# Kernel optimization log

Hardware: AMD Instinct MI355X
Metric: run time of the kernel (lower is better)

The kernel has to match this reference:

```python
import jax, jax.numpy as jnp
import numpy as np

N_STATE = 64
N_OBS = 32
N_IN = 16
T = 1024
DT = 0.01

# Dopri5 Butcher tableau (same as diffrax.Dopri5)
_A_TAB = [
    [],
    [1/5],
    [3/40, 9/40],
    [44/45, -56/15, 32/9],
    [19372/6561, -25360/2187, 64448/6561, -212/729],
    [9017/3168, -355/33, 46732/5247, 49/176, -5103/18656],
    [35/384, 0.0, 500/1113, 125/192, -2187/6784, 11/84],
]
_C_TAB = [0.0, 1/5, 3/10, 4/5, 8/9, 1.0, 1.0]
_B_TAB = [35/384, 0.0, 500/1113, 125/192, -2187/6784, 11/84, 0.0]


def setup_inputs() -> dict:
    key = jax.random.key(0)
    ks = jax.random.split(key, 6)
    ts = jnp.arange(T, dtype=jnp.float32) * DT
    ys = jax.random.normal(ks[0], (T, N_OBS), jnp.float32)
    us = jax.random.normal(ks[1], (T, N_IN), jnp.float32)
    # stable system matrix so the Riccati ODE stays bounded
    A = 0.1 * jax.random.normal(ks[2], (N_STATE, N_STATE), jnp.float32) - jnp.eye(N_STATE, dtype=jnp.float32)
    B = 0.1 * jax.random.normal(ks[3], (N_STATE, N_IN), jnp.float32)
    C = 0.1 * jax.random.normal(ks[4], (N_OBS, N_STATE), jnp.float32)
    x0 = jax.random.normal(ks[5], (N_STATE,), jnp.float32)
    P0 = jnp.eye(N_STATE, dtype=jnp.float32)
    Q = 0.01 * jnp.eye(N_STATE, dtype=jnp.float32)
    R = 0.1 * jnp.eye(N_OBS, dtype=jnp.float32)
    return {"ts": ts, "ys": ys, "us": us, "A": A, "B": B, "C": C,
            "x0": x0, "P0": P0, "Q": Q, "R": R}


def reference(ts, ys, us, A, B, C, x0, P0, Q, R):
    h = ts[1] - ts[0]  # constant step == save spacing (dt0)
    nT = ys.shape[0]
    Rinv = jnp.linalg.inv(R)  # R is constant; original inverts it each rhs eval
    Ct = C.T

    def interp(arr, t):
        # linear interpolation on the uniform grid ts
        s = (t - ts[0]) / h
        i0 = jnp.clip(jnp.floor(s).astype(jnp.int32), 0, nT - 2)
        w = s - i0.astype(s.dtype)
        return arr[i0] * (1.0 - w) + arr[i0 + 1] * w

    def rhs(t, x, P):
        PCtRi = P @ Ct @ Rinv                      # Kalman gain K, [n,p]
        dP = A @ P + P @ A.T + Q - PCtRi @ (C @ P)  # Riccati ODE
        dx = A @ x + B @ interp(us, t) + PCtRi @ (interp(ys, t) - C @ x)
        return dx, dP

    def step(carry, t):
        x, P = carry
        kx, kP = [], []
        for i in range(7):  # fixed 7-stage RK, unrolled
            xi, Pi = x, P
            for j, aij in enumerate(_A_TAB[i]):
                if aij != 0.0:
                    xi = xi + (h * aij) * kx[j]
                    Pi = Pi + (h * aij) * kP[j]
            dx, dP = rhs(t + _C_TAB[i] * h, xi, Pi)
            kx.append(dx)
            kP.append(dP)
        xn, Pn = x, P
        for i, bi in enumerate(_B_TAB):
            if bi != 0.0:
                xn = xn + (h * bi) * kx[i]
                Pn = Pn + (h * bi) * kP[i]
        return (xn, Pn), xn

    (_, _), xs = jax.lax.scan(step, (x0, P0), ts[:-1])
    return jnp.concatenate([x0[None], xs], axis=0)  # [T, n] filtered states
```

## Files before the change

### kernel.cpp

```cpp
#include <hip/hip_runtime.h>

typedef float f32x4 __attribute__((ext_vector_type(4)));
typedef short s16x8 __attribute__((ext_vector_type(8)));
typedef short s16x4 __attribute__((ext_vector_type(4)));

namespace kf {
constexpr int TN = 1024, NS = 64, NO = 32, NI = 16;
constexpr int PP = 72;
constexpr int PK = 40;
constexpr int PKP = 72;

constexpr float ATAB[6][5] = {
  {0.f,0.f,0.f,0.f,0.f},
  {(float)(1.0/5.0),0.f,0.f,0.f,0.f},
  {(float)(3.0/40.0),(float)(9.0/40.0),0.f,0.f,0.f},
  {(float)(44.0/45.0),(float)(-56.0/15.0),(float)(32.0/9.0),0.f,0.f},
  {(float)(19372.0/6561.0),(float)(-25360.0/2187.0),(float)(64448.0/6561.0),(float)(-212.0/729.0),0.f},
  {(float)(9017.0/3168.0),(float)(-355.0/33.0),(float)(46732.0/5247.0),(float)(49.0/176.0),(float)(-5103.0/18656.0)},
};
constexpr float CTAB[6] = {0.f,(float)(1.0/5.0),(float)(3.0/10.0),(float)(4.0/5.0),(float)(8.0/9.0),1.f};
constexpr float BW0=(float)(35.0/384.0), BW2=(float)(500.0/1113.0), BW3=(float)(125.0/192.0),
                BW4=(float)(-2187.0/6784.0), BW5=(float)(11.0/84.0);

struct ShB {
  unsigned short Pib[64*PP];
  unsigned short Ab [64*PP];
  unsigned short Cb [32*PP];
  unsigned short RCb[32*PP];
  unsigned short KKb[64*PK];
  unsigned short GTb[64*PK];
  float Bf[64*16];
  float XV[2][64];
  float CXR[32];
  float BUB[2][64];
  float FAC[32];
  int HYP;
};
constexpr size_t SH_BASE  = (sizeof(ShB) + 255) & ~size_t(255);
constexpr size_t SH_TOTAL = SH_BASE + size_t(5*64*PKP)*4;
}
using namespace kf;

__device__ inline float bf2f(unsigned short u){
  unsigned int x = ((unsigned int)u) << 16; return __builtin_bit_cast(float, x);
}
__device__ inline unsigned short f2bf(float f){
  unsigned int x = __builtin_bit_cast(unsigned int, f);
  return (unsigned short)((x + 0x7fffu + ((x >> 16) & 1u)) >> 16);
}
__device__ inline unsigned int pack2bf(float a, float b){
  return (unsigned int)f2bf(a) | ((unsigned int)f2bf(b) << 16);
}
__device__ inline s16x8 load_frag(const unsigned short* arr, int pitch, int row0, int k0, int hyp){
  const int l = (int)(threadIdx.x & 63), lc = l & 15, lg = l >> 4;
  const unsigned short* p = arr + (row0 + lc) * pitch + k0;
  if ((hyp & 1) == 0) {
    return *(const s16x8*)(p + lg * 8);
  } else {
    s16x4 a = *(const s16x4*)(p + lg * 4);
    s16x4 b = *(const s16x4*)(p + 16 + lg * 4);
    s16x8 r; r[0]=a[0]; r[1]=a[1]; r[2]=a[2]; r[3]=a[3]; r[4]=b[0]; r[5]=b[1]; r[6]=b[2]; r[7]=b[3];
    return r;
  }
}
__device__ inline f32x4 MF(s16x8 a, s16x8 b, f32x4 c, int hyp){
  if (hyp & 2) return __builtin_amdgcn_mfma_f32_16x16x32_bf16(b, a, c, 0, 0, 0);
  return __builtin_amdgcn_mfma_f32_16x16x32_bf16(a, b, c, 0, 0, 0);
}
template<int HYP>
__device__ __forceinline__ s16x8 load_fragT(const unsigned short* arr, int pitch, int row0, int k0){
  const int l = (int)(threadIdx.x & 63), lc = l & 15, lg = l >> 4;
  const unsigned short* p = arr + (row0 + lc) * pitch + k0;
  if constexpr ((HYP & 1) == 0) {
    return *(const s16x8*)(p + lg * 8);
  } else {
    s16x4 a = *(const s16x4*)(p + lg * 4);
    s16x4 b = *(const s16x4*)(p + 16 + lg * 4);
    s16x8 r; r[0]=a[0]; r[1]=a[1]; r[2]=a[2]; r[3]=a[3]; r[4]=b[0]; r[5]=b[1]; r[6]=b[2]; r[7]=b[3];
    return r;
  }
}
template<int HYP>
__device__ __forceinline__ f32x4 MFT(s16x8 a, s16x8 b, f32x4 c){
  if constexpr ((HYP & 2) != 0) return __builtin_amdgcn_mfma_f32_16x16x32_bf16(b, a, c, 0, 0, 0);
  else                          return __builtin_amdgcn_mfma_f32_16x16x32_bf16(a, b, c, 0, 0, 0);
}
__device__ inline float dot8(s16x8 v, f32x4 a, f32x4 b){
  return bf2f(v[0])*a.x + bf2f(v[1])*a.y + bf2f(v[2])*a.z + bf2f(v[3])*a.w
       + bf2f(v[4])*b.x + bf2f(v[5])*b.y + bf2f(v[6])*b.z + bf2f(v[7])*b.w;
}
__device__ inline float dot4bf(s16x4 v, f32x4 a){
  return bf2f(v[0])*a.x + bf2f(v[1])*a.y + bf2f(v[2])*a.z + bf2f(v[3])*a.w;
}

template<int HYP>
__device__ __forceinline__ void scan_body(ShB& sh, float* __restrict__ KPL,
    const float* __restrict__ ts, const float* __restrict__ ys, const float* __restrict__ us,
    const float* __restrict__ x0g, const float* __restrict__ P0g, const float* __restrict__ Qg,
    float* __restrict__ out)
{
  const int tid = (int)threadIdx.x;
  const int w = tid >> 6, l = tid & 63;
  const int lc = l & 15, lg = l >> 4;
  const int sr = w & 3, ch = w >> 2;
  const int xrow = tid >> 3, xpart = tid & 7;
  const int cq = tid >> 4, cpart = tid & 15;

  const float h = ts[1] - ts[0];
  f32x4 z4 = {0.f,0.f,0.f,0.f};
  f32x4 Pfr[2], Qfr[2], APd[2], APT[2];
  s16x8 aA[2], aRC[2], aC[2];
  float XRr, kx0=0.f,kx1=0.f,kx2=0.f,kx3=0.f,kx4=0.f;
  float y1, y2;
  #pragma unroll
  for (int c2 = 0; c2 < 2; ++c2) { Pfr[c2]=z4; Qfr[c2]=z4; APd[c2]=z4; APT[c2]=z4; }

  #pragma unroll
  for (int c2 = 0; c2 < 2; ++c2)
    #pragma unroll
    for (int r = 0; r < 4; ++r) {
      int row = 16*sr + 4*lg + r, col = 16*(2*ch + c2) + lc;
      Pfr[c2][r] = P0g[row*64 + col];
      Qfr[c2][r] = Qg [row*64 + col];
    }
  #pragma unroll
  for (int kb = 0; kb < 2; ++kb) {
    aA [kb] = load_fragT<HYP>(sh.Ab,  PP, 16*sr, 32*kb);
    aRC[kb] = load_fragT<HYP>(sh.RCb, PP, 16*ch, 32*kb);
    aC [kb] = load_fragT<HYP>(sh.Cb,  PP, 16*ch, 32*kb);
  }
  XRr = x0g[xrow];
  if (tid < 64) {
    out[tid] = x0g[tid];
    const f32x4* bf4 = (const f32x4*)&sh.Bf[tid*16];
    const f32x4* up4 = (const f32x4*)us;
    float bu = 0.f;
    #pragma unroll
    for (int m4 = 0; m4 < 4; ++m4) {
      f32x4 b = bf4[m4], u = up4[m4];
      bu += b.x*u.x + b.y*u.y + b.z*u.z + b.w*u.w;
    }
    sh.BUB[0][tid] = bu;
  }
  y1 = ys[cq]; y2 = ys[NO + cq];
  __syncthreads();

  for (int t = 0; t < TN - 1; ++t) {
    #pragma unroll
    for (int st = 0; st < 6; ++st) {
      const int par = st & 1, prv = par ^ 1;
      if (t > 0 || st > 0) {
        float kx;
        {
          s16x8 a0 = *(const s16x8*)&sh.Ab[xrow*PP + 8*xpart];
          f32x4 xa = *(const f32x4*)&sh.XV[prv][8*xpart];
          f32x4 xb = *(const f32x4*)&sh.XV[prv][8*xpart + 4];
          kx = dot8(a0, xa, xb);
          s16x4 kkv = *(const s16x4*)&sh.KKb[xrow*PK + 4*xpart];
          f32x4 cxv = *(const f32x4*)&sh.CXR[4*xpart];
          kx += dot4bf(kkv, cxv);
        }
        kx += __shfl_xor(kx, 1);
        kx += __shfl_xor(kx, 2);
        kx += __shfl_xor(kx, 4);
        if (st == 0) {
          kx += sh.BUB[t & 1][xrow];
        } else {
          const float cp = CTAB[st-1];
          kx += (1.f - cp) * sh.BUB[t & 1][xrow] + cp * sh.BUB[(t + 1) & 1][xrow];
        }
        if (st == 0) {
          float xn = XRr + h*(BW0*kx0 + BW2*kx2 + BW3*kx3 + BW4*kx4 + BW5*kx);
          XRr = xn;
          if (xpart == 0) { out[t*64 + xrow] = xn; sh.XV[par][xrow] = xn; }
        } else {
          float xi = XRr + (h * ATAB[st][st-1]) * kx;
          if (st >= 2 && ATAB[st][0] != 0.f) xi += (h * ATAB[st][0]) * kx0;
          if (st >= 3 && ATAB[st][1] != 0.f) xi += (h * ATAB[st][1]) * kx1;
          if (st >= 4 && ATAB[st][2] != 0.f) xi += (h * ATAB[st][2]) * kx2;
          if (st >= 5 && ATAB[st][3] != 0.f) xi += (h * ATAB[st][3]) * kx3;
          if (st == 1) kx0 = kx; else if (st == 2) kx1 = kx;
          else if (st == 3) kx2 = kx; else if (st == 4) kx3 = kx; else kx4 = kx;
          if (xpart == 0) sh.XV[par][xrow] = xi;
        }
      } else {
        if (xpart == 0) sh.XV[0][xrow] = XRr;
      }
      if (t > 0 || st > 0) {
        s16x8 am = load_fragT<HYP>(sh.KKb, PK, 16*sr, 0);
        #pragma unroll
        for (int c2 = 0; c2 < 2; ++c2) {
          const int ct = 2*ch + c2;
          s16x8 bg = load_fragT<HYP>(sh.GTb, PK, 16*ct, 0);
          f32x4 M = MFT<HYP>(am, bg, z4);
          f32x4 kPv;
          #pragma unroll
          for (int r = 0; r < 4; ++r) kPv[r] = APd[c2][r] + APT[c2][r] - M[r];
          float* kbase = &KPL[(size_t)(16*ct + lc) * PKP + 16*sr + 4*lg];
          f32x4 x;
          if (st == 0) {
            f32x4 k0v = *(const f32x4*)(kbase + 0*64*PKP);
            f32x4 k2v = *(const f32x4*)(kbase + 2*64*PKP);
            f32x4 k3v = *(const f32x4*)(kbase + 3*64*PKP);
            f32x4 k4v = *(const f32x4*)(kbase + 4*64*PKP);
            #pragma unroll
            for (int r = 0; r < 4; ++r)
              Pfr[c2][r] += h * (BW0*k0v[r] + BW2*k2v[r] + BW3*k3v[r]
                               + BW4*k4v[r] + BW5*kPv[r] + Qfr[c2][r]);
            x = Pfr[c2];
          } else {
            *(f32x4*)(kbase + (size_t)(st-1)*64*PKP) = kPv;
            #pragma unroll
            for (int r = 0; r < 4; ++r)
              x[r] = Pfr[c2][r] + (h * CTAB[st]) * Qfr[c2][r] + (h * ATAB[st][st-1]) * kPv[r];
            if (st >= 2) { f32x4 kv = *(const f32x4*)(kbase + 0*64*PKP);
              #pragma unroll
              for (int r = 0; r < 4; ++r) x[r] += (h * ATAB[st][0]) * kv[r]; }
            if (st >= 3) { f32x4 kv = *(const f32x4*)(kbase + 1*64*PKP);
              #pragma unroll
              for (int r = 0; r < 4; ++r) x[r] += (h * ATAB[st][1]) * kv[r]; }
            if (st >= 4) { f32x4 kv = *(const f32x4*)(kbase + 2*64*PKP);
              #pragma unroll
              for (int r = 0; r < 4; ++r) x[r] += (h * ATAB[st][2]) * kv[r]; }
            if (st >= 5) { f32x4 kv = *(const f32x4*)(kbase + 3*64*PKP);
              #pragma unroll
              for (int r = 0; r < 4; ++r) x[r] += (h * ATAB[st][3]) * kv[r]; }
          }
          uint2 pk; pk.x = pack2bf(x[0], x[1]); pk.y = pack2bf(x[2], x[3]);
          *(uint2*)&sh.Pib[(16*ct + lc)*PP + 16*sr + 4*lg] = pk;
        }
      } else {
        #pragma unroll
        for (int c2 = 0; c2 < 2; ++c2) {
          const int ct = 2*ch + c2;
          uint2 pk; pk.x = pack2bf(Pfr[c2][0], Pfr[c2][1]); pk.y = pack2bf(Pfr[c2][2], Pfr[c2][3]);
          *(uint2*)&sh.Pib[(16*ct + lc)*PP + 16*sr + 4*lg] = pk;
        }
      }
      __syncthreads();
      {
        s16x8 aPi0 = load_fragT<HYP>(sh.Pib, PP, 16*sr, 0);
        s16x8 aPi1 = load_fragT<HYP>(sh.Pib, PP, 16*sr, 32);
        #pragma unroll
        for (int c2 = 0; c2 < 2; ++c2) {
          const int ct = 2*ch + c2;
          s16x8 bP0 = load_fragT<HYP>(sh.Pib, PP, 16*ct, 0);
          s16x8 bP1 = load_fragT<HYP>(sh.Pib, PP, 16*ct, 32);
          s16x8 bA0 = load_fragT<HYP>(sh.Ab,  PP, 16*ct, 0);
          s16x8 bA1 = load_fragT<HYP>(sh.Ab,  PP, 16*ct, 32);
          APd[c2] = MFT<HYP>(aA[1], bP1, MFT<HYP>(aA[0], bP0, z4));
          APT[c2] = MFT<HYP>(aPi1, bA1, MFT<HYP>(aPi0, bA0, z4));
        }
        f32x4 aK = MFT<HYP>(aRC[1], aPi1, MFT<HYP>(aRC[0], aPi0, z4));
        uint2 pkk; pkk.x = pack2bf(aK[0], aK[1]); pkk.y = pack2bf(aK[2], aK[3]);
        *(uint2*)&sh.KKb[(16*sr + lc)*PK + 16*ch + 4*lg] = pkk;
        f32x4 aG = MFT<HYP>(aC[1], aPi1, MFT<HYP>(aC[0], aPi0, z4));
        uint2 pkg; pkg.x = pack2bf(aG[0], aG[1]); pkg.y = pack2bf(aG[2], aG[3]);
        *(uint2*)&sh.GTb[(16*sr + lc)*PK + 16*ch + 4*lg] = pkg;
      }
      {
        s16x4 cvv = *(const s16x4*)&sh.Cb[cq*PP + 4*cpart];
        f32x4 xv = *(const f32x4*)&sh.XV[par][4*cpart];
        float cx = dot4bf(cvv, xv);
        cx += __shfl_xor(cx, 1);
        cx += __shfl_xor(cx, 2);
        cx += __shfl_xor(cx, 4);
        cx += __shfl_xor(cx, 8);
        if (cpart == 0) {
          float yc = (1.f - CTAB[st]) * y1 + CTAB[st] * y2;
          sh.CXR[cq] = yc - cx;
        }
      }
      if (st == 0 && tid < 64) {
        const f32x4* bf4 = (const f32x4*)&sh.Bf[tid*16];
        const f32x4* up4 = (const f32x4*)(us + (size_t)(t + 1)*NI);
        float bu = 0.f;
        #pragma unroll
        for (int m4 = 0; m4 < 4; ++m4) {
          f32x4 b = bf4[m4], u = up4[m4];
          bu += b.x*u.x + b.y*u.y + b.z*u.z + b.w*u.w;
        }
        sh.BUB[(t + 1) & 1][tid] = bu;
      }
      __syncthreads();
    }
    y1 = y2;
    if (t + 2 < TN) y2 = ys[(size_t)(t + 2)*NO + cq];
  }

  {
    constexpr int tb = (TN - 1) & 1;
    float kx;
    {
      s16x8 a0 = *(const s16x8*)&sh.Ab[xrow*PP + 8*xpart];
      f32x4 xa = *(const f32x4*)&sh.XV[1][8*xpart];
      f32x4 xb = *(const f32x4*)&sh.XV[1][8*xpart + 4];
      kx = dot8(a0, xa, xb);
      s16x4 kkv = *(const s16x4*)&sh.KKb[xrow*PK + 4*xpart];
      f32x4 cxv = *(const f32x4*)&sh.CXR[4*xpart];
      kx += dot4bf(kkv, cxv);
    }
    kx += __shfl_xor(kx, 1);
    kx += __shfl_xor(kx, 2);
    kx += __shfl_xor(kx, 4);
    kx += sh.BUB[tb][xrow];
    if (xpart == 0) {
      float xn = XRr + h*(BW0*kx0 + BW2*kx2 + BW3*kx3 + BW4*kx4 + BW5*kx);
      out[(TN - 1)*64 + xrow] = xn;
    }
  }
}

__global__ __launch_bounds__(512, 1)
void kf_mfma8(const float* __restrict__ ts, const float* __restrict__ ys,
              const float* __restrict__ us, const float* __restrict__ Ag,
              const float* __restrict__ Bg, const float* __restrict__ Cg,
              const float* __restrict__ x0g, const float* __restrict__ P0g,
              const float* __restrict__ Qg, const float* __restrict__ Rg,
              float* __restrict__ out)
{
  extern __shared__ char dsm[];
  ShB& sh = *(ShB*)dsm;
  float* KPL = (float*)(dsm + SH_BASE);
  float* GJ  = KPL;
  const int tid = (int)threadIdx.x;
  const int wv = tid >> 6;
  const int lc = tid & 15, lg = (tid & 63) >> 4;

  for (int idx = tid; idx < 64*64; idx += 512) sh.Ab[(idx>>6)*PP + (idx&63)] = f2bf(Ag[idx]);
  for (int idx = tid; idx < 32*64; idx += 512) sh.Cb[(idx>>6)*PP + (idx&63)] = f2bf(Cg[idx]);
  for (int idx = tid; idx < 64*16; idx += 512) sh.Bf[idx] = Bg[idx];
  for (int idx = tid; idx < 32*64; idx += 512) {
    int r = idx >> 6, c = idx & 63;
    GJ[idx] = (c < 32) ? Rg[r*32 + c] : ((c - 32) == r ? 1.f : 0.f);
  }
  __syncthreads();
  for (int k2 = 0; k2 < 32; ++k2) {
    if (tid < 32) sh.FAC[tid] = GJ[tid*64 + k2];
    __syncthreads();
    const float pinv = 1.f / sh.FAC[k2];
    float oldv[4], vk[4];
    #pragma unroll
    for (int s = 0; s < 4; ++s) {
      int idx = tid + s*512;
      oldv[s] = GJ[idx];
      vk[s]   = GJ[k2*64 + (idx & 63)];
    }
    __syncthreads();
    #pragma unroll
    for (int s = 0; s < 4; ++s) {
      int idx = tid + s*512, i = idx >> 6;
      GJ[idx] = (i == k2) ? (oldv[s] * pinv) : (oldv[s] - sh.FAC[i] * (vk[s] * pinv));
    }
    __syncthreads();
  }
  for (int idx = tid; idx < 32*64; idx += 512) {
    int q = idx >> 6, k = idx & 63;
    float a = 0.f;
    for (int p = 0; p < 32; ++p) a += GJ[q*64 + 32 + p] * Cg[p*64 + k];
    sh.RCb[q*PP + k] = f2bf(a);
  }
  __syncthreads();
  __shared__ float Xref[256];
  if (tid < 256) {
    int r = tid >> 4, c = tid & 15;
    float a = 0.f;
    for (int k = 0; k < 32; ++k) a += bf2f(sh.Ab[r*PP + k]) * bf2f(sh.Ab[(16 + c)*PP + k]);
    Xref[tid] = a;
  }
  if (tid == 0) sh.HYP = -1;
  __syncthreads();
  for (int hh = 0; hh < 4; ++hh) {
    if (wv == 0) {
      s16x8 af = load_frag(sh.Ab, PP, 0, 0, hh);
      s16x8 bf = load_frag(sh.Ab, PP, 16, 0, hh);
      f32x4 z = {0.f,0.f,0.f,0.f};
      f32x4 d = MF(af, bf, z, hh);
      int ok = 1;
      #pragma unroll
      for (int r = 0; r < 4; ++r) {
        float rf = Xref[(lg*4 + r)*16 + lc];
        ok &= (fabsf(d[r] - rf) <= 1e-3f + 1e-2f * fabsf(rf)) ? 1 : 0;
      }
      if (__all(ok) && tid == 0) { if (sh.HYP < 0) sh.HYP = hh; }
    }
    __syncthreads();
  }
  const int sHyp = (sh.HYP < 0) ? 0 : sh.HYP;

  switch (sHyp) {
    case 0: scan_body<0>(sh, KPL, ts, ys, us, x0g, P0g, Qg, out); break;
    case 1: scan_body<1>(sh, KPL, ts, ys, us, x0g, P0g, Qg, out); break;
    case 2: scan_body<2>(sh, KPL, ts, ys, us, x0g, P0g, Qg, out); break;
    default: scan_body<3>(sh, KPL, ts, ys, us, x0g, P0g, Qg, out); break;
  }
}

extern "C" void kernel_launch(void* const* d_in, const int* in_sizes, int n_in,
                              void* d_out, int out_size, void* d_ws, size_t ws_size,
                              hipStream_t stream) {
  (void)in_sizes; (void)n_in; (void)out_size; (void)d_ws; (void)ws_size;
  const float* ts  = (const float*)d_in[0];
  const float* ys  = (const float*)d_in[1];
  const float* us  = (const float*)d_in[2];
  const float* A   = (const float*)d_in[3];
  const float* B   = (const float*)d_in[4];
  const float* C   = (const float*)d_in[5];
  const float* x0  = (const float*)d_in[6];
  const float* P0  = (const float*)d_in[7];
  const float* Q   = (const float*)d_in[8];
  const float* R   = (const float*)d_in[9];
  (void)hipFuncSetAttribute(reinterpret_cast<const void*>(kf_mfma8),
                            hipFuncAttributeMaxDynamicSharedMemorySize, (int)SH_TOTAL);
  hipLaunchKernelGGL(kf_mfma8, dim3(1), dim3(512), SH_TOTAL, stream,
                     ts, ys, us, A, B, C, x0, P0, Q, R, (float*)d_out);
}
```

Measured before the change: 8.897 ms.

## Fold state-vector updates into MFMA tiles as an extra padded row of P

```diff
diff --git a/kernel.cpp b/kernel.cpp
--- a/kernel.cpp
+++ b/kernel.cpp
@@ -23,16 +23,15 @@
                 BW4=(float)(-2187.0/6784.0), BW5=(float)(11.0/84.0);
 
 struct ShB {
-  unsigned short Pib[64*PP];
+  unsigned short Pib[80*PP];
   unsigned short Ab [64*PP];
   unsigned short Cb [32*PP];
   unsigned short RCb[32*PP];
   unsigned short KKb[64*PK];
-  unsigned short GTb[64*PK];
+  unsigned short GTb[80*PK];
   float Bf[64*16];
-  float XV[2][64];
-  float CXR[32];
   float BUB[2][64];
+  float KXL[5][64];
   float FAC[32];
   int HYP;
 };
@@ -85,13 +84,6 @@
   if constexpr ((HYP & 2) != 0) return __builtin_amdgcn_mfma_f32_16x16x32_bf16(b, a, c, 0, 0, 0);
   else                          return __builtin_amdgcn_mfma_f32_16x16x32_bf16(a, b, c, 0, 0, 0);
 }
-__device__ inline float dot8(s16x8 v, f32x4 a, f32x4 b){
-  return bf2f(v[0])*a.x + bf2f(v[1])*a.y + bf2f(v[2])*a.z + bf2f(v[3])*a.w
-       + bf2f(v[4])*b.x + bf2f(v[5])*b.y + bf2f(v[6])*b.z + bf2f(v[7])*b.w;
-}
-__device__ inline float dot4bf(s16x4 v, f32x4 a){
-  return bf2f(v[0])*a.x + bf2f(v[1])*a.y + bf2f(v[2])*a.z + bf2f(v[3])*a.w;
-}
 
 template<int HYP>
 __device__ __forceinline__ void scan_body(ShB& sh, float* __restrict__ KPL,
@@ -103,17 +95,18 @@
   const int w = tid >> 6, l = tid & 63;
   const int lc = l & 15, lg = l >> 4;
   const int sr = w & 3, ch = w >> 2;
-  const int xrow = tid >> 3, xpart = tid & 7;
-  const int cq = tid >> 4, cpart = tid & 15;
+  const int rowbase = 16*sr + 4*lg;
+  const bool isx = (ch == 0);
+  const bool isg = (sr == 3);
 
   const float h = ts[1] - ts[0];
   f32x4 z4 = {0.f,0.f,0.f,0.f};
-  f32x4 Pfr[2], Qfr[2], APd[2], APT[2];
-  s16x8 aA[2], aRC[2], aC[2];
-  float XRr, kx0=0.f,kx1=0.f,kx2=0.f,kx3=0.f,kx4=0.f;
-  float y1, y2;
+  f32x4 Pfr[2], Qfr[2], APd[2], APT[2], APdX, XRv;
+  s16x8 aA[2], aRC[2], aC[2], bA[2][2];
+  f32x4 y1v = z4, y2v = z4;
   #pragma unroll
   for (int c2 = 0; c2 < 2; ++c2) { Pfr[c2]=z4; Qfr[c2]=z4; APd[c2]=z4; APT[c2]=z4; }
+  APdX = z4;
 
   #pragma unroll
   for (int c2 = 0; c2 < 2; ++c2)
@@ -128,10 +121,18 @@
     aA [kb] = load_fragT<HYP>(sh.Ab,  PP, 16*sr, 32*kb);
     aRC[kb] = load_fragT<HYP>(sh.RCb, PP, 16*ch, 32*kb);
     aC [kb] = load_fragT<HYP>(sh.Cb,  PP, 16*ch, 32*kb);
-  }
-  XRr = x0g[xrow];
+    #pragma unroll
+    for (int c2 = 0; c2 < 2; ++c2)
+      bA[c2][kb] = load_fragT<HYP>(sh.Ab, PP, 16*(2*ch + c2), 32*kb);
+  }
+  XRv = *(const f32x4*)&x0g[rowbase];
+  if (isg) {
+    y1v = *(const f32x4*)&ys[16*ch + 4*lg];
+    y2v = *(const f32x4*)&ys[NO + 16*ch + 4*lg];
+  }
   if (tid < 64) {
     out[tid] = x0g[tid];
+    sh.Pib[64*PP + tid] = f2bf(x0g[tid]);
     const f32x4* bf4 = (const f32x4*)&sh.Bf[tid*16];
     const f32x4* up4 = (const f32x4*)us;
     float bu = 0.f;
@@ -142,52 +143,17 @@
     }
     sh.BUB[0][tid] = bu;
   }
-  y1 = ys[cq]; y2 = ys[NO + cq];
+  for (int idx = tid; idx < 15*PP; idx += 512) sh.Pib[65*PP + idx] = 0;
+  if (tid < PP - 64) sh.Pib[64*PP + 64 + tid] = 0;
+  for (int idx = tid; idx < 16*PK; idx += 512) sh.GTb[64*PK + idx] = 0;
   __syncthreads();
 
   for (int t = 0; t < TN - 1; ++t) {
     #pragma unroll
     for (int st = 0; st < 6; ++st) {
-      const int par = st & 1, prv = par ^ 1;
+      s16x8 am;
       if (t > 0 || st > 0) {
-        float kx;
-        {
-          s16x8 a0 = *(const s16x8*)&sh.Ab[xrow*PP + 8*xpart];
-          f32x4 xa = *(const f32x4*)&sh.XV[prv][8*xpart];
-          f32x4 xb = *(const f32x4*)&sh.XV[prv][8*xpart + 4];
-          kx = dot8(a0, xa, xb);
-          s16x4 kkv = *(const s16x4*)&sh.KKb[xrow*PK + 4*xpart];
-          f32x4 cxv = *(const f32x4*)&sh.CXR[4*xpart];
-          kx += dot4bf(kkv, cxv);
-        }
-        kx += __shfl_xor(kx, 1);
-        kx += __shfl_xor(kx, 2);
-        kx += __shfl_xor(kx, 4);
-        if (st == 0) {
-          kx += sh.BUB[t & 1][xrow];
-        } else {
-          const float cp = CTAB[st-1];
-          kx += (1.f - cp) * sh.BUB[t & 1][xrow] + cp * sh.BUB[(t + 1) & 1][xrow];
-        }
-        if (st == 0) {
-          float xn = XRr + h*(BW0*kx0 + BW2*kx2 + BW3*kx3 + BW4*kx4 + BW5*kx);
-          XRr = xn;
-          if (xpart == 0) { out[t*64 + xrow] = xn; sh.XV[par][xrow] = xn; }
-        } else {
-          float xi = XRr + (h * ATAB[st][st-1]) * kx;
-          if (st >= 2 && ATAB[st][0] != 0.f) xi += (h * ATAB[st][0]) * kx0;
-          if (st >= 3 && ATAB[st][1] != 0.f) xi += (h * ATAB[st][1]) * kx1;
-          if (st >= 4 && ATAB[st][2] != 0.f) xi += (h * ATAB[st][2]) * kx2;
-          if (st >= 5 && ATAB[st][3] != 0.f) xi += (h * ATAB[st][3]) * kx3;
-          if (st == 1) kx0 = kx; else if (st == 2) kx1 = kx;
-          else if (st == 3) kx2 = kx; else if (st == 4) kx3 = kx; else kx4 = kx;
-          if (xpart == 0) sh.XV[par][xrow] = xi;
-        }
-      } else {
-        if (xpart == 0) sh.XV[0][xrow] = XRr;
-      }
-      if (t > 0 || st > 0) {
-        s16x8 am = load_fragT<HYP>(sh.KKb, PK, 16*sr, 0);
+        am = load_fragT<HYP>(sh.KKb, PK, 16*sr, 0);
         #pragma unroll
         for (int c2 = 0; c2 < 2; ++c2) {
           const int ct = 2*ch + c2;
@@ -229,6 +195,46 @@
           uint2 pk; pk.x = pack2bf(x[0], x[1]); pk.y = pack2bf(x[2], x[3]);
           *(uint2*)&sh.Pib[(16*ct + lc)*PP + 16*sr + 4*lg] = pk;
         }
+        if (isx) {
+          s16x8 bgX = load_fragT<HYP>(sh.GTb, PK, 64, 0);
+          f32x4 MX = MFT<HYP>(am, bgX, z4);
+          f32x4 kx = APdX + MX;
+          {
+            f32x4 bu1 = *(const f32x4*)&sh.BUB[t & 1][rowbase];
+            if (st == 0) {
+              kx += bu1;
+            } else {
+              const float cp = CTAB[st-1];
+              if (cp != 0.f) {
+                f32x4 bu2 = *(const f32x4*)&sh.BUB[(t + 1) & 1][rowbase];
+                kx += (1.f - cp) * bu1 + cp * bu2;
+              } else {
+                kx += bu1;
+              }
+            }
+          }
+          f32x4 xiv;
+          if (st == 0) {
+            f32x4 k0 = *(const f32x4*)&sh.KXL[0][rowbase];
+            f32x4 k2 = *(const f32x4*)&sh.KXL[2][rowbase];
+            f32x4 k3 = *(const f32x4*)&sh.KXL[3][rowbase];
+            f32x4 k4 = *(const f32x4*)&sh.KXL[4][rowbase];
+            XRv += h * (BW0*k0 + BW2*k2 + BW3*k3 + BW4*k4 + BW5*kx);
+            if (lc == 0) *(f32x4*)&out[(size_t)t*64 + rowbase] = XRv;
+            xiv = XRv;
+          } else {
+            if (lc == 0) *(f32x4*)&sh.KXL[st-1][rowbase] = kx;
+            xiv = XRv + (h * ATAB[st][st-1]) * kx;
+            if (st >= 2 && ATAB[st][0] != 0.f) xiv += (h * ATAB[st][0]) * (*(const f32x4*)&sh.KXL[0][rowbase]);
+            if (st >= 3 && ATAB[st][1] != 0.f) xiv += (h * ATAB[st][1]) * (*(const f32x4*)&sh.KXL[1][rowbase]);
+            if (st >= 4 && ATAB[st][2] != 0.f) xiv += (h * ATAB[st][2]) * (*(const f32x4*)&sh.KXL[2][rowbase]);
+            if (st >= 5 && ATAB[st][3] != 0.f) xiv += (h * ATAB[st][3]) * (*(const f32x4*)&sh.KXL[3][rowbase]);
+          }
+          if (lc == 0) {
+            uint2 pk; pk.x = pack2bf(xiv[0], xiv[1]); pk.y = pack2bf(xiv[2], xiv[3]);
+            *(uint2*)&sh.Pib[64*PP + rowbase] = pk;
+          }
+        }
       } else {
         #pragma unroll
         for (int c2 = 0; c2 < 2; ++c2) {
@@ -246,10 +252,8 @@
           const int ct = 2*ch + c2;
           s16x8 bP0 = load_fragT<HYP>(sh.Pib, PP, 16*ct, 0);
           s16x8 bP1 = load_fragT<HYP>(sh.Pib, PP, 16*ct, 32);
-          s16x8 bA0 = load_fragT<HYP>(sh.Ab,  PP, 16*ct, 0);
-          s16x8 bA1 = load_fragT<HYP>(sh.Ab,  PP, 16*ct, 32);
           APd[c2] = MFT<HYP>(aA[1], bP1, MFT<HYP>(aA[0], bP0, z4));
-          APT[c2] = MFT<HYP>(aPi1, bA1, MFT<HYP>(aPi0, bA0, z4));
+          APT[c2] = MFT<HYP>(aPi1, bA[c2][1], MFT<HYP>(aPi0, bA[c2][0], z4));
         }
         f32x4 aK = MFT<HYP>(aRC[1], aPi1, MFT<HYP>(aRC[0], aPi0, z4));
         uint2 pkk; pkk.x = pack2bf(aK[0], aK[1]); pkk.y = pack2bf(aK[2], aK[3]);
@@ -258,17 +262,25 @@
         uint2 pkg; pkg.x = pack2bf(aG[0], aG[1]); pkg.y = pack2bf(aG[2], aG[3]);
         *(uint2*)&sh.GTb[(16*sr + lc)*PK + 16*ch + 4*lg] = pkg;
       }
-      {
-        s16x4 cvv = *(const s16x4*)&sh.Cb[cq*PP + 4*cpart];
-        f32x4 xv = *(const f32x4*)&sh.XV[par][4*cpart];
-        float cx = dot4bf(cvv, xv);
-        cx += __shfl_xor(cx, 1);
-        cx += __shfl_xor(cx, 2);
-        cx += __shfl_xor(cx, 4);
-        cx += __shfl_xor(cx, 8);
-        if (cpart == 0) {
-          float yc = (1.f - CTAB[st]) * y1 + CTAB[st] * y2;
-          sh.CXR[cq] = yc - cx;
+      if (isx || isg) {
+        s16x8 px0 = load_fragT<HYP>(sh.Pib, PP, 64, 0);
+        s16x8 px1 = load_fragT<HYP>(sh.Pib, PP, 64, 32);
+        if (isx) {
+          APdX = MFT<HYP>(aA[1], px1, MFT<HYP>(aA[0], px0, z4));
+        }
+        if (isg) {
+          f32x4 gx = MFT<HYP>(aC[1], px1, MFT<HYP>(aC[0], px0, z4));
+          const float c = CTAB[st];
+          f32x4 v;
+          #pragma unroll
+          for (int r = 0; r < 4; ++r) {
+            float yc = (1.f - c) * y1v[r] + c * y2v[r];
+            v[r] = yc - gx[r];
+          }
+          uint2 pk;
+          if (lc == 0) { pk.x = pack2bf(v[0], v[1]); pk.y = pack2bf(v[2], v[3]); }
+          else         { pk.x = 0u; pk.y = 0u; }
+          *(uint2*)&sh.GTb[(64 + lc)*PK + 16*ch + 4*lg] = pk;
         }
       }
       if (st == 0 && tid < 64) {
@@ -284,35 +296,29 @@
       }
       __syncthreads();
     }
-    y1 = y2;
-    if (t + 2 < TN) y2 = ys[(size_t)(t + 2)*NO + cq];
-  }
-
-  {
-    constexpr int tb = (TN - 1) & 1;
-    float kx;
-    {
-      s16x8 a0 = *(const s16x8*)&sh.Ab[xrow*PP + 8*xpart];
-      f32x4 xa = *(const f32x4*)&sh.XV[1][8*xpart];
-      f32x4 xb = *(const f32x4*)&sh.XV[1][8*xpart + 4];
-      kx = dot8(a0, xa, xb);
-      s16x4 kkv = *(const s16x4*)&sh.KKb[xrow*PK + 4*xpart];
-      f32x4 cxv = *(const f32x4*)&sh.CXR[4*xpart];
-      kx += dot4bf(kkv, cxv);
-    }
-    kx += __shfl_xor(kx, 1);
-    kx += __shfl_xor(kx, 2);
-    kx += __shfl_xor(kx, 4);
-    kx += sh.BUB[tb][xrow];
-    if (xpart == 0) {
-      float xn = XRr + h*(BW0*kx0 + BW2*kx2 + BW3*kx3 + BW4*kx4 + BW5*kx);
-      out[(TN - 1)*64 + xrow] = xn;
-    }
+    if (isg) {
+      y1v = y2v;
+      if (t + 2 < TN) y2v = *(const f32x4*)&ys[(size_t)(t + 2)*NO + 16*ch + 4*lg];
+    }
+  }
+
+  if (isx) {
+    s16x8 am  = load_fragT<HYP>(sh.KKb, PK, 16*sr, 0);
+    s16x8 bgX = load_fragT<HYP>(sh.GTb, PK, 64, 0);
+    f32x4 MX = MFT<HYP>(am, bgX, z4);
+    f32x4 kx = APdX + MX;
+    kx += *(const f32x4*)&sh.BUB[(TN - 1) & 1][rowbase];
+    f32x4 k0 = *(const f32x4*)&sh.KXL[0][rowbase];
+    f32x4 k2 = *(const f32x4*)&sh.KXL[2][rowbase];
+    f32x4 k3 = *(const f32x4*)&sh.KXL[3][rowbase];
+    f32x4 k4 = *(const f32x4*)&sh.KXL[4][rowbase];
+    XRv += h * (BW0*k0 + BW2*k2 + BW3*k3 + BW4*k4 + BW5*kx);
+    if (lc == 0) *(f32x4*)&out[(size_t)(TN - 1)*64 + rowbase] = XRv;
   }
 }
 
 __global__ __launch_bounds__(512, 1)
-void kf_mfma8(const float* __restrict__ ts, const float* __restrict__ ys,
+void kf_mfma9(const float* __restrict__ ts, const float* __restrict__ ys,
               const float* __restrict__ us, const float* __restrict__ Ag,
               const float* __restrict__ Bg, const float* __restrict__ Cg,
               const float* __restrict__ x0g, const float* __restrict__ P0g,
@@ -410,8 +416,8 @@
   const float* P0  = (const float*)d_in[7];
   const float* Q   = (const float*)d_in[8];
   const float* R   = (const float*)d_in[9];
-  (void)hipFuncSetAttribute(reinterpret_cast<const void*>(kf_mfma8),
+  (void)hipFuncSetAttribute(reinterpret_cast<const void*>(kf_mfma9),
                             hipFuncAttributeMaxDynamicSharedMemorySize, (int)SH_TOTAL);
-  hipLaunchKernelGGL(kf_mfma8, dim3(1), dim3(512), SH_TOTAL, stream,
+  hipLaunchKernelGGL(kf_mfma9, dim3(1), dim3(512), SH_TOTAL, stream,
                      ts, ys, us, A, B, C, x0, P0, Q, R, (float*)d_out);
 }
```

Result: faster. 7.367 ms (-17.2%).
